# Kernel optimization log

Hardware: AMD Instinct MI355X
Metric: run time of the kernel (lower is better)

Reference implementation:

```python
import jax, jax.numpy as jnp
import numpy as np

D_MODEL = 1024
NUM_EXPERTS = 8
TOP_K = 2
B, S = 1, 2048


def setup_inputs() -> dict:
    key = jax.random.key(0)
    ks = jax.random.split(key, 8)
    sd = 1.0 / np.sqrt(D_MODEL)
    x = jax.random.normal(ks[0], (B, S, D_MODEL), dtype=jnp.float32)
    gate_w = jax.random.normal(ks[1], (D_MODEL, NUM_EXPERTS), dtype=jnp.float32) * sd
    gate_b = jnp.zeros((NUM_EXPERTS,), dtype=jnp.float32)
    w1 = jax.random.normal(ks[2], (NUM_EXPERTS, D_MODEL, 8 * D_MODEL), dtype=jnp.float32) * sd
    b1 = jnp.zeros((NUM_EXPERTS, 8 * D_MODEL), dtype=jnp.float32)
    w2 = jax.random.normal(ks[3], (NUM_EXPERTS, 4 * D_MODEL, D_MODEL), dtype=jnp.float32) * (1.0 / np.sqrt(4 * D_MODEL))
    b2 = jnp.zeros((NUM_EXPERTS, D_MODEL), dtype=jnp.float32)
    return {"x": x, "gate_w": gate_w, "gate_b": gate_b, "w1": w1, "b1": b1, "w2": w2, "b2": b2}


def reference(x, gate_w, gate_b, w1, b1, w2, b2):
    # Gating: top-k logits, softmax over the selected k
    gate_logits = jnp.einsum('bsd,de->bse', x, gate_w) + gate_b          # [B,S,E]
    weights, indices = jax.lax.top_k(gate_logits, TOP_K)                  # [B,S,K]
    weights = jax.nn.softmax(weights, axis=-1)

    # Dense all-expert compute (matches original masked-sum math; dropout in eval)
    h = jnp.einsum('bsd,edh->ebsh', x, w1) + b1[:, None, None, :]         # [E,B,S,8D]
    xh, gh = jnp.split(h, 2, axis=-1)                                     # each [E,B,S,4D]
    act = jax.nn.silu(gh) * xh
    out_e = jnp.einsum('ebsf,efd->ebsd', act, w2) + b2[:, None, None, :]  # [E,B,S,D]

    # Combine: gather the top-k expert outputs per token and weight-sum
    out_e = jnp.transpose(out_e, (1, 2, 0, 3))                            # [B,S,E,D]
    sel = jnp.take_along_axis(out_e, indices[..., None], axis=2)          # [B,S,K,D]
    return jnp.sum(sel * weights[..., None], axis=2)                      # [B,S,D]
```

## Files before the change

### kernel.cpp

```cpp
#include <hip/hip_runtime.h>
#include <hip/hip_bf16.h>

#define S 2048
#define D 1024
#define NE 8
#define HF 4096
#define HH 8192
#define BK 32
#define ACT_ROWS 4224
#define MAXRB 40

typedef __attribute__((ext_vector_type(8))) __bf16 bf16x8;
typedef __attribute__((ext_vector_type(4))) float f32x4;

__device__ __forceinline__ unsigned cvtpk(float lo, float hi) {
  unsigned r;
  asm("v_cvt_pk_bf16_f32 %0, %1, %2" : "=v"(r) : "v"(lo), "v"(hi));
  return r;
}
__device__ __forceinline__ unsigned bf16b(float f) {
  unsigned b = __float_as_uint(f);
  return (b + 0x7fffu + ((b >> 16) & 1u)) >> 16;
}
__device__ __forceinline__ void gll16(const ushort* g, ushort* l) {
  __builtin_amdgcn_global_load_lds(
      (const __attribute__((address_space(1))) void*)g,
      (__attribute__((address_space(3))) void*)l, 16, 0, 0);
}

__device__ __forceinline__ void transpose_body(const float* __restrict__ Sp,
                                               ushort* __restrict__ Dp, int R, int C,
                                               int n0, int k0, unsigned* __restrict__ L) {
  const int t = threadIdx.x;
  const int l32 = t & 31;
  const int pgrp = t >> 5;
#pragma unroll
  for (int r = 0; r < 8; ++r) {
    const int pp = r * 8 + pgrp;
    const int ka = k0 + 2 * pp;
    const float4 a = *(const float4*)(Sp + (size_t)ka * C + n0 + l32 * 4);
    const float4 b = *(const float4*)(Sp + (size_t)(ka + 1) * C + n0 + l32 * 4);
    uint4 v = {cvtpk(a.x, b.x), cvtpk(a.y, b.y), cvtpk(a.z, b.z), cvtpk(a.w, b.w)};
    *(uint4*)&L[pp * 128 + l32 * 4] = v;
  }
  __syncthreads();
  const int n_l = t >> 1;
  const int h = t & 1;
  unsigned vv[32];
#pragma unroll
  for (int p = 0; p < 32; ++p) vv[p] = L[(h * 32 + p) * 128 + n_l];
  ushort* drow = Dp + (size_t)(n0 + n_l) * R + k0 + h * 64;
#pragma unroll
  for (int q = 0; q < 8; ++q) ((uint4*)drow)[q] = *(uint4*)&vv[q * 4];
}

union PrepSmem {
  unsigned tr[64 * 128];
  float sm[4][NE];
};

__global__ __launch_bounds__(256) void prep_kernel(
    const float* __restrict__ w1, ushort* __restrict__ w1t,
    const float* __restrict__ w2, ushort* __restrict__ w2t,
    const float* __restrict__ x, const float* __restrict__ gw,
    const float* __restrict__ gb, ushort* __restrict__ xb,
    int* __restrict__ mi0, int* __restrict__ mi1,
    float* __restrict__ mw0, float* __restrict__ mw1) {
  __shared__ PrepSmem u;
  const int id = blockIdx.x;
  if (id < 4096) {
    const int e = id >> 9;
    const int rem = id & 511;
    transpose_body(w1 + (size_t)e * D * HH, w1t + (size_t)e * D * HH, D, HH,
                   (rem & 63) * 128, (rem >> 6) * 128, u.tr);
    return;
  }
  if (id < 6144) {
    const int id2 = id - 4096;
    const int e = id2 >> 8;
    const int rem = id2 & 255;
    transpose_body(w2 + (size_t)e * HF * D, w2t + (size_t)e * HF * D, HF, D,
                   (rem & 7) * 128, (rem >> 3) * 128, u.tr);
    return;
  }
  const int t = id - 6144;
  const int l = threadIdx.x;
  const float4 xv = ((const float4*)(x + (size_t)t * D))[l];
  uint2 wv = {cvtpk(xv.x, xv.y), cvtpk(xv.z, xv.w)};
  ((uint2*)(xb + (size_t)t * D))[l] = wv;

  float xa[4] = {xv.x, xv.y, xv.z, xv.w};
  float acc[NE];
#pragma unroll
  for (int e = 0; e < NE; ++e) acc[e] = 0.f;
  const float* g0 = gw + (size_t)(4 * l) * NE;
#pragma unroll
  for (int j = 0; j < 4; ++j)
#pragma unroll
    for (int e = 0; e < NE; ++e) acc[e] += xa[j] * g0[j * NE + e];
#pragma unroll
  for (int e = 0; e < NE; ++e) {
    float v = acc[e];
#pragma unroll
    for (int off = 32; off > 0; off >>= 1) v += __shfl_xor(v, off);
    acc[e] = v;
  }
  const int wid = l >> 6;
  if ((l & 63) == 0) {
#pragma unroll
    for (int e = 0; e < NE; ++e) u.sm[wid][e] = acc[e];
  }
  __syncthreads();
  if (l == 0) {
    float lg[NE];
#pragma unroll
    for (int e = 0; e < NE; ++e)
      lg[e] = u.sm[0][e] + u.sm[1][e] + u.sm[2][e] + u.sm[3][e] + gb[e];
    int i0 = 0; float m0 = lg[0];
#pragma unroll
    for (int e = 1; e < NE; ++e) if (lg[e] > m0) { m0 = lg[e]; i0 = e; }
    int i1 = -1; float m1 = -3.4e38f;
#pragma unroll
    for (int e = 0; e < NE; ++e) if (e != i0 && lg[e] > m1) { m1 = lg[e]; i1 = e; }
    float p = __expf(m1 - m0);
    float inv = 1.f / (1.f + p);
    mi0[t] = i0; mi1[t] = i1;
    mw0[t] = inv; mw1[t] = p * inv;
  }
}

__global__ __launch_bounds__(1024) void route_kernel(
    const int* __restrict__ mi0, const int* __restrict__ mi1,
    int* __restrict__ counts, int* __restrict__ basep, int* __restrict__ list_tok,
    int* __restrict__ mr0, int* __restrict__ mr1,
    int* __restrict__ rb_e, int* __restrict__ rb_row0, int* __restrict__ rb_n) {
  __shared__ int cnt[NE];
  __shared__ int cur[NE];
  const int t = threadIdx.x;
  if (t < NE) cnt[t] = 0;
  __syncthreads();
  const int e0a = mi0[t], e1a = mi1[t];
  const int e0b = mi0[t + 1024], e1b = mi1[t + 1024];
  atomicAdd(&cnt[e0a], 1); atomicAdd(&cnt[e1a], 1);
  atomicAdd(&cnt[e0b], 1); atomicAdd(&cnt[e1b], 1);
  __syncthreads();
  if (t == 0) {
    int s = 0;
#pragma unroll
    for (int e = 0; e < NE; ++e) { basep[e] = s; cur[e] = s; s += cnt[e]; }
    basep[NE] = s;
    int nrb = 0;
    for (int e = 0; e < NE; ++e)
      for (int r0 = 0; r0 < cnt[e]; r0 += 128) {
        rb_e[nrb] = e; rb_row0[nrb] = r0; ++nrb;
      }
    *rb_n = nrb;
  }
  if (t < NE) counts[t] = cnt[t];
  __syncthreads();
  int r;
  r = atomicAdd(&cur[e0a], 1); list_tok[r] = t; mr0[t] = r;
  r = atomicAdd(&cur[e1a], 1); list_tok[r] = t; mr1[t] = r;
  r = atomicAdd(&cur[e0b], 1); list_tok[r] = t + 1024; mr0[t + 1024] = r;
  r = atomicAdd(&cur[e1b], 1); list_tok[r] = t + 1024; mr1[t + 1024] = r;
}

__global__ __launch_bounds__(256) void gemm1_kernel(
    const ushort* __restrict__ xb, const ushort* __restrict__ w1t,
    const float* __restrict__ b1, const int* __restrict__ counts,
    const int* __restrict__ basep, const int* __restrict__ list_tok,
    const int* __restrict__ rb_e, const int* __restrict__ rb_row0,
    const int* __restrict__ rb_n, ushort* __restrict__ act_buf) {
  const int rb = blockIdx.y;
  if (rb >= *rb_n) return;
  const int e = rb_e[rb];
  const int row0 = rb_row0[rb];
  const int cnt = counts[e];
  const int jt = blockIdx.x * 64;
  const ushort* __restrict__ W = w1t + (size_t)e * D * HH;
  const int gbase = basep[e];

  __shared__ ushort As[2][128][BK];
  __shared__ ushort Bs[2][128][BK];

  const int tid = threadIdx.x;
  const int w = tid >> 6;
  const int i = tid & 63;

  const int rA0 = w * 32 + (i >> 2);
  const int rA1 = rA0 + 16;
  int s0 = row0 + rA0; if (s0 >= cnt) s0 = cnt - 1;
  int s1 = row0 + rA1; if (s1 >= cnt) s1 = cnt - 1;
  const ushort* pa0 = xb + (size_t)list_tok[gbase + s0] * D + (i & 3) * 8;
  const ushort* pa1 = xb + (size_t)list_tok[gbase + s1] * D + (i & 3) * 8;
  const ushort* pb0 = W + ((size_t)(rA0 >> 6) * HF + jt + (rA0 & 63)) * D + (i & 3) * 8;
  const ushort* pb1 = W + ((size_t)(rA1 >> 6) * HF + jt + (rA1 & 63)) * D + (i & 3) * 8;

  const int wm = (w >> 1) * 64;
  const int wn = (w & 1) * 32;
  const int lr = i & 15;
  const int kg = i >> 4;

  f32x4 acc[2][4][2] = {};

  gll16(pa0, &As[0][w * 32][0]);
  gll16(pa1, &As[0][w * 32 + 16][0]);
  gll16(pb0, &Bs[0][w * 32][0]);
  gll16(pb1, &Bs[0][w * 32 + 16][0]);
  __syncthreads();

  int cur = 0;
#pragma unroll 1
  for (int it = 0; it < D / BK; ++it) {
    if (it + 1 < D / BK) {
      const int ko = (it + 1) * BK;
      gll16(pa0 + ko, &As[cur ^ 1][w * 32][0]);
      gll16(pa1 + ko, &As[cur ^ 1][w * 32 + 16][0]);
      gll16(pb0 + ko, &Bs[cur ^ 1][w * 32][0]);
      gll16(pb1 + ko, &Bs[cur ^ 1][w * 32 + 16][0]);
    }
    bf16x8 af[4], bfr[2][2];
#pragma unroll
    for (int mi = 0; mi < 4; ++mi)
      af[mi] = *(const bf16x8*)&As[cur][wm + mi * 16 + lr][kg * 8];
#pragma unroll
    for (int h = 0; h < 2; ++h)
#pragma unroll
      for (int ni = 0; ni < 2; ++ni)
        bfr[h][ni] = *(const bf16x8*)&Bs[cur][h * 64 + wn + ni * 16 + lr][kg * 8];
#pragma unroll
    for (int h = 0; h < 2; ++h)
#pragma unroll
      for (int mi = 0; mi < 4; ++mi)
#pragma unroll
        for (int ni = 0; ni < 2; ++ni)
          acc[h][mi][ni] = __builtin_amdgcn_mfma_f32_16x16x32_bf16(af[mi], bfr[h][ni],
                                                                   acc[h][mi][ni], 0, 0, 0);
    __syncthreads();
    cur ^= 1;
  }

#pragma unroll
  for (int mi = 0; mi < 4; ++mi)
#pragma unroll
    for (int ni = 0; ni < 2; ++ni) {
      const int c = jt + wn + ni * 16 + lr;
      const float bx = b1[(size_t)e * HH + c];
      const float bg = b1[(size_t)e * HH + HF + c];
      f32x4 vx = acc[0][mi][ni];
      f32x4 vg = acc[1][mi][ni];
#pragma unroll
      for (int q = 0; q < 4; ++q) {
        const int slot = row0 + wm + mi * 16 + kg * 4 + q;
        if (slot < cnt) {
          float xv = vx[q] + bx;
          float g = vg[q] + bg;
          float a = g / (1.f + __expf(-g)) * xv;
          act_buf[(size_t)(gbase + slot) * HF + c] = (ushort)bf16b(a);
        }
      }
    }
}

__global__ __launch_bounds__(256) void gemm2_kernel(
    const ushort* __restrict__ act_buf, const ushort* __restrict__ w2t,
    const int* __restrict__ counts, const int* __restrict__ basep,
    const int* __restrict__ rb_e, const int* __restrict__ rb_row0,
    const int* __restrict__ rb_n, ushort* __restrict__ oe) {
  const int rb = blockIdx.y;
  if (rb >= *rb_n) return;
  const int e = rb_e[rb];
  const int row0 = rb_row0[rb];
  const int cnt = counts[e];
  const int split = blockIdx.z;
  const int jt = blockIdx.x * 128;
  const ushort* __restrict__ W = w2t + (size_t)e * HF * D;
  const int gbase = basep[e];

  __shared__ ushort As[2][128][BK];
  __shared__ ushort Bs[2][128][BK];

  const int tid = threadIdx.x;
  const int w = tid >> 6;
  const int i = tid & 63;

  const int r0 = w * 32 + (i >> 2);
  const size_t kbase = (size_t)split * (HF / 2);
  const ushort* pa0 = act_buf + (size_t)(gbase + row0 + r0) * HF + kbase + (i & 3) * 8;
  const ushort* pa1 = pa0 + (size_t)16 * HF;
  const ushort* pb0 = W + (size_t)(jt + r0) * HF + kbase + (i & 3) * 8;
  const ushort* pb1 = pb0 + (size_t)16 * HF;

  const int wm = (w >> 1) * 64;
  const int wn = (w & 1) * 64;
  const int lr = i & 15;
  const int kg = i >> 4;

  f32x4 acc[4][4] = {};

  gll16(pa0, &As[0][w * 32][0]);
  gll16(pa1, &As[0][w * 32 + 16][0]);
  gll16(pb0, &Bs[0][w * 32][0]);
  gll16(pb1, &Bs[0][w * 32 + 16][0]);
  __syncthreads();

  int cur = 0;
#pragma unroll 1
  for (int it = 0; it < (HF / 2) / BK; ++it) {
    if (it + 1 < (HF / 2) / BK) {
      const int ko = (it + 1) * BK;
      gll16(pa0 + ko, &As[cur ^ 1][w * 32][0]);
      gll16(pa1 + ko, &As[cur ^ 1][w * 32 + 16][0]);
      gll16(pb0 + ko, &Bs[cur ^ 1][w * 32][0]);
      gll16(pb1 + ko, &Bs[cur ^ 1][w * 32 + 16][0]);
    }
    bf16x8 af[4], bfr[4];
#pragma unroll
    for (int mi = 0; mi < 4; ++mi)
      af[mi] = *(const bf16x8*)&As[cur][wm + mi * 16 + lr][kg * 8];
#pragma unroll
    for (int ni = 0; ni < 4; ++ni)
      bfr[ni] = *(const bf16x8*)&Bs[cur][wn + ni * 16 + lr][kg * 8];
#pragma unroll
    for (int mi = 0; mi < 4; ++mi)
#pragma unroll
      for (int ni = 0; ni < 4; ++ni)
        acc[mi][ni] = __builtin_amdgcn_mfma_f32_16x16x32_bf16(af[mi], bfr[ni],
                                                              acc[mi][ni], 0, 0, 0);
    __syncthreads();
    cur ^= 1;
  }

#pragma unroll
  for (int mi = 0; mi < 4; ++mi)
#pragma unroll
    for (int ni = 0; ni < 4; ++ni) {
      f32x4 v = acc[mi][ni];
#pragma unroll
      for (int q = 0; q < 4; ++q) {
        const int slot = row0 + wm + mi * 16 + kg * 4 + q;
        if (slot < cnt)
          oe[((size_t)split * ACT_ROWS + gbase + slot) * D + jt + wn + ni * 16 + lr] =
              (ushort)bf16b(v[q]);
      }
    }
}

__global__ void combine_kernel(const ushort* __restrict__ oe,
                               const int* __restrict__ mr0, const int* __restrict__ mr1,
                               const float* __restrict__ mw0, const float* __restrict__ mw1,
                               const int* __restrict__ mi0, const int* __restrict__ mi1,
                               const float* __restrict__ b2, float* __restrict__ out) {
  const int t = blockIdx.x;
  const int l = threadIdx.x;
  const float w0 = mw0[t], w1 = mw1[t];
  const int r0 = mr0[t], r1 = mr1[t];
  float a0[4] = {0.f, 0.f, 0.f, 0.f}, a1[4] = {0.f, 0.f, 0.f, 0.f};
#pragma unroll
  for (int s = 0; s < 2; ++s) {
    uint2 u0 = *(const uint2*)(oe + ((size_t)s * ACT_ROWS + r0) * D + l * 4);
    uint2 u1 = *(const uint2*)(oe + ((size_t)s * ACT_ROWS + r1) * D + l * 4);
    a0[0] += __uint_as_float(u0.x << 16);
    a0[1] += __uint_as_float(u0.x & 0xffff0000u);
    a0[2] += __uint_as_float(u0.y << 16);
    a0[3] += __uint_as_float(u0.y & 0xffff0000u);
    a1[0] += __uint_as_float(u1.x << 16);
    a1[1] += __uint_as_float(u1.x & 0xffff0000u);
    a1[2] += __uint_as_float(u1.y << 16);
    a1[3] += __uint_as_float(u1.y & 0xffff0000u);
  }
  float4 c0 = ((const float4*)(b2 + (size_t)mi0[t] * D))[l];
  float4 c1 = ((const float4*)(b2 + (size_t)mi1[t] * D))[l];
  float4 r;
  r.x = w0 * (a0[0] + c0.x) + w1 * (a1[0] + c1.x);
  r.y = w0 * (a0[1] + c0.y) + w1 * (a1[1] + c1.y);
  r.z = w0 * (a0[2] + c0.z) + w1 * (a1[2] + c1.z);
  r.w = w0 * (a0[3] + c0.w) + w1 * (a1[3] + c1.w);
  ((float4*)(out + (size_t)t * D))[l] = r;
}

extern "C" void kernel_launch(void* const* d_in, const int* in_sizes, int n_in,
                              void* d_out, int out_size, void* d_ws, size_t ws_size,
                              hipStream_t stream) {
  const float* x  = (const float*)d_in[0];
  const float* gw = (const float*)d_in[1];
  const float* gb = (const float*)d_in[2];
  const float* w1 = (const float*)d_in[3];
  const float* b1 = (const float*)d_in[4];
  const float* w2 = (const float*)d_in[5];
  const float* b2 = (const float*)d_in[6];
  float* out = (float*)d_out;

  char* ws = (char*)d_ws;
  int*   counts   = (int*)(ws + 0);
  int*   basep    = (int*)(ws + 64);
  int*   rb_n     = (int*)(ws + 128);
  int*   rb_e     = (int*)(ws + 192);
  int*   rb_row0  = (int*)(ws + 384);
  int*   mi0      = (int*)(ws + 1024);
  int*   mi1      = (int*)(ws + 1024 + 1 * 8192);
  int*   mr0      = (int*)(ws + 1024 + 2 * 8192);
  int*   mr1      = (int*)(ws + 1024 + 3 * 8192);
  float* mw0      = (float*)(ws + 1024 + 4 * 8192);
  float* mw1      = (float*)(ws + 1024 + 5 * 8192);
  int*   list_tok = (int*)(ws + 1024 + 6 * 8192);
  ushort* xb      = (ushort*)(ws + 66560);
  ushort* act_buf = (ushort*)(ws + 4260864);
  ushort* oe      = (ushort*)(ws + 38863872);
  ushort* w1t     = (ushort*)(ws + 73466880);
  ushort* w2t     = (ushort*)(ws + 207684608);

  prep_kernel<<<4096 + 2048 + S, 256, 0, stream>>>(w1, w1t, w2, w2t, x, gw, gb, xb,
                                                   mi0, mi1, mw0, mw1);
  route_kernel<<<1, 1024, 0, stream>>>(mi0, mi1, counts, basep, list_tok, mr0, mr1,
                                       rb_e, rb_row0, rb_n);
  gemm1_kernel<<<dim3(64, MAXRB), 256, 0, stream>>>(xb, w1t, b1, counts, basep, list_tok,
                                                    rb_e, rb_row0, rb_n, act_buf);
  gemm2_kernel<<<dim3(8, MAXRB, 2), 256, 0, stream>>>(act_buf, w2t, counts, basep,
                                                      rb_e, rb_row0, rb_n, oe);
  combine_kernel<<<S, 256, 0, stream>>>(oe, mr0, mr1, mw0, mw1, mi0, mi1, b2, out);
}
```

Baseline: 320.7 us.

## Fuse fp32 weight conversion into GEMM B-tile loads, drop prep transpose pass

Removes the separate prep pass that transposed and converted all expert weights to bf16 each call. The GEMM kernels now load fp32 weight rows directly, pack pairs of k rows into bf16 with cvt_pk, and store them in a k-major padded LDS layout read back as MFMA fragments. This avoids writing and re-reading a full bf16 weight copy, but each weight tile is re-read in fp32 by every row block of an expert and converted redundantly. It also adds register-staged prefetch in place of async global-to-LDS loads, and LDS reads become four scalar loads per fragment.

```diff
diff --git a/kernel.cpp b/kernel.cpp
--- a/kernel.cpp
+++ b/kernel.cpp
@@ -28,62 +28,12 @@
       (__attribute__((address_space(3))) void*)l, 16, 0, 0);
 }
 
-__device__ __forceinline__ void transpose_body(const float* __restrict__ Sp,
-                                               ushort* __restrict__ Dp, int R, int C,
-                                               int n0, int k0, unsigned* __restrict__ L) {
-  const int t = threadIdx.x;
-  const int l32 = t & 31;
-  const int pgrp = t >> 5;
-#pragma unroll
-  for (int r = 0; r < 8; ++r) {
-    const int pp = r * 8 + pgrp;
-    const int ka = k0 + 2 * pp;
-    const float4 a = *(const float4*)(Sp + (size_t)ka * C + n0 + l32 * 4);
-    const float4 b = *(const float4*)(Sp + (size_t)(ka + 1) * C + n0 + l32 * 4);
-    uint4 v = {cvtpk(a.x, b.x), cvtpk(a.y, b.y), cvtpk(a.z, b.z), cvtpk(a.w, b.w)};
-    *(uint4*)&L[pp * 128 + l32 * 4] = v;
-  }
-  __syncthreads();
-  const int n_l = t >> 1;
-  const int h = t & 1;
-  unsigned vv[32];
-#pragma unroll
-  for (int p = 0; p < 32; ++p) vv[p] = L[(h * 32 + p) * 128 + n_l];
-  ushort* drow = Dp + (size_t)(n0 + n_l) * R + k0 + h * 64;
-#pragma unroll
-  for (int q = 0; q < 8; ++q) ((uint4*)drow)[q] = *(uint4*)&vv[q * 4];
-}
-
-union PrepSmem {
-  unsigned tr[64 * 128];
-  float sm[4][NE];
-};
-
-__global__ __launch_bounds__(256) void prep_kernel(
-    const float* __restrict__ w1, ushort* __restrict__ w1t,
-    const float* __restrict__ w2, ushort* __restrict__ w2t,
+__global__ __launch_bounds__(256) void gate_kernel(
     const float* __restrict__ x, const float* __restrict__ gw,
     const float* __restrict__ gb, ushort* __restrict__ xb,
     int* __restrict__ mi0, int* __restrict__ mi1,
     float* __restrict__ mw0, float* __restrict__ mw1) {
-  __shared__ PrepSmem u;
-  const int id = blockIdx.x;
-  if (id < 4096) {
-    const int e = id >> 9;
-    const int rem = id & 511;
-    transpose_body(w1 + (size_t)e * D * HH, w1t + (size_t)e * D * HH, D, HH,
-                   (rem & 63) * 128, (rem >> 6) * 128, u.tr);
-    return;
-  }
-  if (id < 6144) {
-    const int id2 = id - 4096;
-    const int e = id2 >> 8;
-    const int rem = id2 & 255;
-    transpose_body(w2 + (size_t)e * HF * D, w2t + (size_t)e * HF * D, HF, D,
-                   (rem & 7) * 128, (rem >> 3) * 128, u.tr);
-    return;
-  }
-  const int t = id - 6144;
+  const int t = blockIdx.x;
   const int l = threadIdx.x;
   const float4 xv = ((const float4*)(x + (size_t)t * D))[l];
   uint2 wv = {cvtpk(xv.x, xv.y), cvtpk(xv.z, xv.w)};
@@ -105,17 +55,18 @@
     for (int off = 32; off > 0; off >>= 1) v += __shfl_xor(v, off);
     acc[e] = v;
   }
+  __shared__ float sm[4][NE];
   const int wid = l >> 6;
   if ((l & 63) == 0) {
 #pragma unroll
-    for (int e = 0; e < NE; ++e) u.sm[wid][e] = acc[e];
+    for (int e = 0; e < NE; ++e) sm[wid][e] = acc[e];
   }
   __syncthreads();
   if (l == 0) {
     float lg[NE];
 #pragma unroll
     for (int e = 0; e < NE; ++e)
-      lg[e] = u.sm[0][e] + u.sm[1][e] + u.sm[2][e] + u.sm[3][e] + gb[e];
+      lg[e] = sm[0][e] + sm[1][e] + sm[2][e] + sm[3][e] + gb[e];
     int i0 = 0; float m0 = lg[0];
 #pragma unroll
     for (int e = 1; e < NE; ++e) if (lg[e] > m0) { m0 = lg[e]; i0 = e; }
@@ -166,7 +117,7 @@
 }
 
 __global__ __launch_bounds__(256) void gemm1_kernel(
-    const ushort* __restrict__ xb, const ushort* __restrict__ w1t,
+    const ushort* __restrict__ xb, const float* __restrict__ w1,
     const float* __restrict__ b1, const int* __restrict__ counts,
     const int* __restrict__ basep, const int* __restrict__ list_tok,
     const int* __restrict__ rb_e, const int* __restrict__ rb_row0,
@@ -177,11 +128,11 @@
   const int row0 = rb_row0[rb];
   const int cnt = counts[e];
   const int jt = blockIdx.x * 64;
-  const ushort* __restrict__ W = w1t + (size_t)e * D * HH;
+  const float* __restrict__ Wf = w1 + (size_t)e * D * HH;
   const int gbase = basep[e];
 
   __shared__ ushort As[2][128][BK];
-  __shared__ ushort Bs[2][128][BK];
+  __shared__ unsigned Bs[2][32][68];
 
   const int tid = threadIdx.x;
   const int w = tid >> 6;
@@ -193,8 +144,11 @@
   int s1 = row0 + rA1; if (s1 >= cnt) s1 = cnt - 1;
   const ushort* pa0 = xb + (size_t)list_tok[gbase + s0] * D + (i & 3) * 8;
   const ushort* pa1 = xb + (size_t)list_tok[gbase + s1] * D + (i & 3) * 8;
-  const ushort* pb0 = W + ((size_t)(rA0 >> 6) * HF + jt + (rA0 & 63)) * D + (i & 3) * 8;
-  const ushort* pb1 = W + ((size_t)(rA1 >> 6) * HF + jt + (rA1 & 63)) * D + (i & 3) * 8;
+
+  const int kp = tid >> 4;
+  const int n4 = (tid & 15) * 4;
+  const float* pBx = Wf + (size_t)(2 * kp) * HH + jt + n4;
+  const float* pBg = pBx + HF;
 
   const int wm = (w >> 1) * 64;
   const int wn = (w & 1) * 32;
@@ -203,21 +157,34 @@
 
   f32x4 acc[2][4][2] = {};
 
+  {
+    float4 x0 = *(const float4*)(pBx);
+    float4 x1 = *(const float4*)(pBx + HH);
+    float4 g0 = *(const float4*)(pBg);
+    float4 g1 = *(const float4*)(pBg + HH);
+    uint4 ux = {cvtpk(x0.x, x1.x), cvtpk(x0.y, x1.y), cvtpk(x0.z, x1.z), cvtpk(x0.w, x1.w)};
+    uint4 ug = {cvtpk(g0.x, g1.x), cvtpk(g0.y, g1.y), cvtpk(g0.z, g1.z), cvtpk(g0.w, g1.w)};
+    *(uint4*)&Bs[0][kp][n4] = ux;
+    *(uint4*)&Bs[0][16 + kp][n4] = ug;
+  }
   gll16(pa0, &As[0][w * 32][0]);
   gll16(pa1, &As[0][w * 32 + 16][0]);
-  gll16(pb0, &Bs[0][w * 32][0]);
-  gll16(pb1, &Bs[0][w * 32 + 16][0]);
   __syncthreads();
 
   int cur = 0;
 #pragma unroll 1
   for (int it = 0; it < D / BK; ++it) {
-    if (it + 1 < D / BK) {
+    const bool pf = (it + 1 < D / BK);
+    float4 x0, x1, g0, g1;
+    if (pf) {
+      const size_t koff = (size_t)(it + 1) * BK * HH;
+      x0 = *(const float4*)(pBx + koff);
+      x1 = *(const float4*)(pBx + koff + HH);
+      g0 = *(const float4*)(pBg + koff);
+      g1 = *(const float4*)(pBg + koff + HH);
       const int ko = (it + 1) * BK;
       gll16(pa0 + ko, &As[cur ^ 1][w * 32][0]);
       gll16(pa1 + ko, &As[cur ^ 1][w * 32 + 16][0]);
-      gll16(pb0 + ko, &Bs[cur ^ 1][w * 32][0]);
-      gll16(pb1 + ko, &Bs[cur ^ 1][w * 32 + 16][0]);
     }
     bf16x8 af[4], bfr[2][2];
 #pragma unroll
@@ -226,8 +193,15 @@
 #pragma unroll
     for (int h = 0; h < 2; ++h)
 #pragma unroll
-      for (int ni = 0; ni < 2; ++ni)
-        bfr[h][ni] = *(const bf16x8*)&Bs[cur][h * 64 + wn + ni * 16 + lr][kg * 8];
+      for (int ni = 0; ni < 2; ++ni) {
+        const int col = wn + ni * 16 + lr;
+        uint4 tv;
+        tv.x = Bs[cur][h * 16 + kg * 4 + 0][col];
+        tv.y = Bs[cur][h * 16 + kg * 4 + 1][col];
+        tv.z = Bs[cur][h * 16 + kg * 4 + 2][col];
+        tv.w = Bs[cur][h * 16 + kg * 4 + 3][col];
+        bfr[h][ni] = *(const bf16x8*)&tv;
+      }
 #pragma unroll
     for (int h = 0; h < 2; ++h)
 #pragma unroll
@@ -236,6 +210,12 @@
         for (int ni = 0; ni < 2; ++ni)
           acc[h][mi][ni] = __builtin_amdgcn_mfma_f32_16x16x32_bf16(af[mi], bfr[h][ni],
                                                                    acc[h][mi][ni], 0, 0, 0);
+    if (pf) {
+      uint4 ux = {cvtpk(x0.x, x1.x), cvtpk(x0.y, x1.y), cvtpk(x0.z, x1.z), cvtpk(x0.w, x1.w)};
+      uint4 ug = {cvtpk(g0.x, g1.x), cvtpk(g0.y, g1.y), cvtpk(g0.z, g1.z), cvtpk(g0.w, g1.w)};
+      *(uint4*)&Bs[cur ^ 1][kp][n4] = ux;
+      *(uint4*)&Bs[cur ^ 1][16 + kp][n4] = ug;
+    }
     __syncthreads();
     cur ^= 1;
   }
@@ -263,7 +243,7 @@
 }
 
 __global__ __launch_bounds__(256) void gemm2_kernel(
-    const ushort* __restrict__ act_buf, const ushort* __restrict__ w2t,
+    const ushort* __restrict__ act_buf, const float* __restrict__ w2,
     const int* __restrict__ counts, const int* __restrict__ basep,
     const int* __restrict__ rb_e, const int* __restrict__ rb_row0,
     const int* __restrict__ rb_n, ushort* __restrict__ oe) {
@@ -274,22 +254,25 @@
   const int cnt = counts[e];
   const int split = blockIdx.z;
   const int jt = blockIdx.x * 128;
-  const ushort* __restrict__ W = w2t + (size_t)e * HF * D;
+  const float* __restrict__ Wf = w2 + (size_t)e * HF * D;
   const int gbase = basep[e];
+  const size_t kbase = (size_t)split * (HF / 2);
 
   __shared__ ushort As[2][128][BK];
-  __shared__ ushort Bs[2][128][BK];
+  __shared__ unsigned Bs[2][16][132];
 
   const int tid = threadIdx.x;
   const int w = tid >> 6;
   const int i = tid & 63;
 
-  const int r0 = w * 32 + (i >> 2);
-  const size_t kbase = (size_t)split * (HF / 2);
-  const ushort* pa0 = act_buf + (size_t)(gbase + row0 + r0) * HF + kbase + (i & 3) * 8;
+  const int rA0 = w * 32 + (i >> 2);
+  const ushort* pa0 = act_buf + (size_t)(gbase + row0 + rA0) * HF + kbase + (i & 3) * 8;
   const ushort* pa1 = pa0 + (size_t)16 * HF;
-  const ushort* pb0 = W + (size_t)(jt + r0) * HF + kbase + (i & 3) * 8;
-  const ushort* pb1 = pb0 + (size_t)16 * HF;
+
+  const int grp = tid >> 5;
+  const int n4 = (tid & 31) * 4;
+  const float* pB0 = Wf + (kbase + 2 * grp) * D + jt + n4;
+  const float* pB1 = pB0 + (size_t)16 * D;
 
   const int wm = (w >> 1) * 64;
   const int wn = (w & 1) * 64;
@@ -298,35 +281,61 @@
 
   f32x4 acc[4][4] = {};
 
+  {
+    float4 a0 = *(const float4*)(pB0);
+    float4 a1 = *(const float4*)(pB0 + D);
+    float4 c0 = *(const float4*)(pB1);
+    float4 c1 = *(const float4*)(pB1 + D);
+    uint4 u0 = {cvtpk(a0.x, a1.x), cvtpk(a0.y, a1.y), cvtpk(a0.z, a1.z), cvtpk(a0.w, a1.w)};
+    uint4 u1 = {cvtpk(c0.x, c1.x), cvtpk(c0.y, c1.y), cvtpk(c0.z, c1.z), cvtpk(c0.w, c1.w)};
+    *(uint4*)&Bs[0][grp][n4] = u0;
+    *(uint4*)&Bs[0][8 + grp][n4] = u1;
+  }
   gll16(pa0, &As[0][w * 32][0]);
   gll16(pa1, &As[0][w * 32 + 16][0]);
-  gll16(pb0, &Bs[0][w * 32][0]);
-  gll16(pb1, &Bs[0][w * 32 + 16][0]);
   __syncthreads();
 
   int cur = 0;
 #pragma unroll 1
   for (int it = 0; it < (HF / 2) / BK; ++it) {
-    if (it + 1 < (HF / 2) / BK) {
+    const bool pf = (it + 1 < (HF / 2) / BK);
+    float4 a0, a1, c0, c1;
+    if (pf) {
+      const size_t koff = (size_t)(it + 1) * BK * D;
+      a0 = *(const float4*)(pB0 + koff);
+      a1 = *(const float4*)(pB0 + koff + D);
+      c0 = *(const float4*)(pB1 + koff);
+      c1 = *(const float4*)(pB1 + koff + D);
       const int ko = (it + 1) * BK;
       gll16(pa0 + ko, &As[cur ^ 1][w * 32][0]);
       gll16(pa1 + ko, &As[cur ^ 1][w * 32 + 16][0]);
-      gll16(pb0 + ko, &Bs[cur ^ 1][w * 32][0]);
-      gll16(pb1 + ko, &Bs[cur ^ 1][w * 32 + 16][0]);
     }
     bf16x8 af[4], bfr[4];
 #pragma unroll
     for (int mi = 0; mi < 4; ++mi)
       af[mi] = *(const bf16x8*)&As[cur][wm + mi * 16 + lr][kg * 8];
 #pragma unroll
-    for (int ni = 0; ni < 4; ++ni)
-      bfr[ni] = *(const bf16x8*)&Bs[cur][wn + ni * 16 + lr][kg * 8];
+    for (int ni = 0; ni < 4; ++ni) {
+      const int col = wn + ni * 16 + lr;
+      uint4 tv;
+      tv.x = Bs[cur][kg * 4 + 0][col];
+      tv.y = Bs[cur][kg * 4 + 1][col];
+      tv.z = Bs[cur][kg * 4 + 2][col];
+      tv.w = Bs[cur][kg * 4 + 3][col];
+      bfr[ni] = *(const bf16x8*)&tv;
+    }
 #pragma unroll
     for (int mi = 0; mi < 4; ++mi)
 #pragma unroll
       for (int ni = 0; ni < 4; ++ni)
         acc[mi][ni] = __builtin_amdgcn_mfma_f32_16x16x32_bf16(af[mi], bfr[ni],
                                                               acc[mi][ni], 0, 0, 0);
+    if (pf) {
+      uint4 u0 = {cvtpk(a0.x, a1.x), cvtpk(a0.y, a1.y), cvtpk(a0.z, a1.z), cvtpk(a0.w, a1.w)};
+      uint4 u1 = {cvtpk(c0.x, c1.x), cvtpk(c0.y, c1.y), cvtpk(c0.z, c1.z), cvtpk(c0.w, c1.w)};
+      *(uint4*)&Bs[cur ^ 1][grp][n4] = u0;
+      *(uint4*)&Bs[cur ^ 1][8 + grp][n4] = u1;
+    }
     __syncthreads();
     cur ^= 1;
   }
@@ -407,16 +416,13 @@
   ushort* xb      = (ushort*)(ws + 66560);
   ushort* act_buf = (ushort*)(ws + 4260864);
   ushort* oe      = (ushort*)(ws + 38863872);
-  ushort* w1t     = (ushort*)(ws + 73466880);
-  ushort* w2t     = (ushort*)(ws + 207684608);
-
-  prep_kernel<<<4096 + 2048 + S, 256, 0, stream>>>(w1, w1t, w2, w2t, x, gw, gb, xb,
-                                                   mi0, mi1, mw0, mw1);
+
+  gate_kernel<<<S, 256, 0, stream>>>(x, gw, gb, xb, mi0, mi1, mw0, mw1);
   route_kernel<<<1, 1024, 0, stream>>>(mi0, mi1, counts, basep, list_tok, mr0, mr1,
                                        rb_e, rb_row0, rb_n);
-  gemm1_kernel<<<dim3(64, MAXRB), 256, 0, stream>>>(xb, w1t, b1, counts, basep, list_tok,
+  gemm1_kernel<<<dim3(64, MAXRB), 256, 0, stream>>>(xb, w1, b1, counts, basep, list_tok,
                                                     rb_e, rb_row0, rb_n, act_buf);
-  gemm2_kernel<<<dim3(8, MAXRB, 2), 256, 0, stream>>>(act_buf, w2t, counts, basep,
+  gemm2_kernel<<<dim3(8, MAXRB, 2), 256, 0, stream>>>(act_buf, w2, counts, basep,
                                                       rb_e, rb_row0, rb_n, oe);
   combine_kernel<<<S, 256, 0, stream>>>(oe, mr0, mr1, mw0, mw1, mi0, mi1, b2, out);
 }
```

Measured after the change: 266.1 us. -17.0%, faster.
